# Kernel optimization log

Hardware: AMD Instinct MI355X
Metric: run time of the kernel (lower is better)

## Reference

```python
import jax, jax.numpy as jnp
import numpy as np

B, N, C, H = 8, 1024, 1024, 16


def setup_inputs() -> dict:
    key = jax.random.key(0)
    k1, k2, k3 = jax.random.split(key, 3)
    x = jax.random.normal(k1, (B, N, C), dtype=jnp.float32)
    # torch Linear weights stored pre-transposed as [in, out]
    w_qkv = jax.random.normal(k2, (C, 3 * C), dtype=jnp.float32) * (1.0 / np.sqrt(C))
    scale = jnp.ones((H, 1, 1), dtype=jnp.float32)
    w_out = jax.random.normal(k3, (C, C), dtype=jnp.float32) * (1.0 / np.sqrt(C))
    b_out = jnp.zeros((C,), dtype=jnp.float32)
    return {"x": x, "w_qkv": w_qkv, "scale": scale, "w_out": w_out, "b_out": b_out}


def _masked_softmax(dots, allow):
    # allow: [N, N] bool; True where attention is permitted (strictly lower triangle).
    neg = jnp.finfo(dots.dtype).min
    logits = jnp.where(allow, dots, neg)
    rowmax = jnp.max(logits, axis=-1, keepdims=True)
    unnorm = jnp.where(allow, jnp.exp(logits - rowmax), 0.0)
    denom = jnp.sum(unnorm, axis=-1, keepdims=True)
    # fully-masked rows (row 0) -> all-zero attention (flash-attn convention)
    return unnorm / jnp.where(denom == 0, 1.0, denom)


def reference(x, w_qkv, scale, w_out, b_out):
    b, n, c = x.shape
    h = scale.shape[0]
    d = c // h
    qkv = x @ w_qkv                                   # [B, N, 3C]
    q, k, v = jnp.split(qkv, 3, axis=-1)
    def heads(t):
        return t.reshape(b, n, h, d).transpose(0, 2, 1, 3)  # [B, H, N, D]
    q, k, v = heads(q), heads(k), heads(v)
    dots = jnp.einsum("bhnd,bhmd->bhnm", q, k) * scale     # per-head learnable scale
    # mask upper triangle AND the diagonal: allow only j < i
    allow = jnp.tril(jnp.ones((n, n), dtype=bool), k=-1)
    attn = _masked_softmax(dots, allow)
    out = jnp.einsum("bhnm,bhmd->bhnd", attn, v)           # [B, H, N, D]
    out = out.transpose(0, 2, 1, 3).reshape(b, n, c)
    return out @ w_out + b_out
```

## Files before the change

### kernel.cpp

```cpp
#include <hip/hip_runtime.h>

#define B_ 8
#define N_ 1024
#define C_ 1024
#define H_ 16
#define D_ 64

typedef __attribute__((ext_vector_type(8))) short short8v;
typedef __attribute__((ext_vector_type(4))) float f32x4;
typedef __attribute__((ext_vector_type(4))) unsigned short ushort4v;

__device__ __forceinline__ unsigned short f2bf_rne(float f) {
    unsigned int u = __float_as_uint(f);
    u += 0x7FFFu + ((u >> 16) & 1u);
    return (unsigned short)(u >> 16);
}
__device__ __forceinline__ float bf2f(unsigned short h) {
    return __uint_as_float(((unsigned int)h) << 16);
}

__global__ __launch_bounds__(256) void convert_transpose(
    const float* __restrict__ W, unsigned short* __restrict__ T_hi,
    unsigned short* __restrict__ T_lo, int K, int N)
{
    __shared__ float tile[32][33];
    const int nb = blockIdx.x * 32, kb = blockIdx.y * 32;
    const int t = threadIdx.x;
    {
        const int kr = t >> 3, nq = (t & 7) * 4;
        const float4 v = *(const float4*)&W[(size_t)(kb + kr) * N + nb + nq];
        tile[kr][nq + 0] = v.x; tile[kr][nq + 1] = v.y;
        tile[kr][nq + 2] = v.z; tile[kr][nq + 3] = v.w;
    }
    __syncthreads();
    {
        const int nr = t >> 3, kq = (t & 7) * 4;
        ushort4v hv, lv;
#pragma unroll
        for (int j = 0; j < 4; ++j) {
            const float f = tile[kq + j][nr];
            const unsigned short hu = f2bf_rne(f);
            hv[j] = hu;
            lv[j] = f2bf_rne(f - bf2f(hu));
        }
        const size_t o = (size_t)(nb + nr) * K + kb + kq;
        *(ushort4v*)&T_hi[o] = hv;
        *(ushort4v*)&T_lo[o] = lv;
    }
}

template<int A_F32>
__global__ __launch_bounds__(256, 2) void gemm_bf16x3(
    const void* __restrict__ Asrc, const unsigned short* __restrict__ Alo_src,
    const unsigned short* __restrict__ Bt_hi,
    const unsigned short* __restrict__ Bt_lo,
    const float* __restrict__ bias, float* __restrict__ Cmat,
    int M, int N, int K)
{
    __shared__ short As_hi[128 * 32], As_lo[128 * 32];
    __shared__ short Bs_hi[128 * 32], Bs_lo[128 * 32];

    const int tid = threadIdx.x;
    const int lane = tid & 63;
    const int wave = tid >> 6;
    const int wm = wave >> 1, wn = wave & 1;
    const int bm = blockIdx.y * 128, bn = blockIdx.x * 128;
    const int l15 = lane & 15, l4 = lane >> 4;

    f32x4 acc[4][4];
#pragma unroll
    for (int m = 0; m < 4; ++m)
#pragma unroll
        for (int n = 0; n < 4; ++n) acc[m][n] = (f32x4){0.f, 0.f, 0.f, 0.f};

    for (int k0 = 0; k0 < K; k0 += 32) {
        if (A_F32) {
            const float* A = (const float*)Asrc;
#pragma unroll
            for (int c = 0; c < 4; ++c) {
                const int u = tid + 256 * c;
                const int row = u >> 3, kc = u & 7;
                const float4 v = *(const float4*)&A[(size_t)(bm + row) * K + k0 + kc * 4];
                const float fv[4] = {v.x, v.y, v.z, v.w};
                ushort4v hv, lv;
#pragma unroll
                for (int j = 0; j < 4; ++j) {
                    const unsigned short hu = f2bf_rne(fv[j]);
                    hv[j] = hu;
                    lv[j] = f2bf_rne(fv[j] - bf2f(hu));
                }
                const int off = (row * 64 + kc * 8) ^ ((row & 7) << 4);
                *(ushort4v*)((char*)As_hi + off) = hv;
                *(ushort4v*)((char*)As_lo + off) = lv;
            }
        } else {
            const unsigned short* Ah = (const unsigned short*)Asrc;
#pragma unroll
            for (int c = 0; c < 2; ++c) {
                const int u = tid + 256 * c;
                const int row = u >> 2, kg = u & 3;
                const size_t gg = (size_t)(bm + row) * K + k0 + kg * 8;
                const int off = (row * 64 + kg * 16) ^ ((row & 7) << 4);
                *(short8v*)((char*)As_hi + off) = *(const short8v*)&Ah[gg];
                *(short8v*)((char*)As_lo + off) = *(const short8v*)&Alo_src[gg];
            }
        }
#pragma unroll
        for (int c = 0; c < 2; ++c) {
            const int u = tid + 256 * c;
            const int row = u >> 2, kg = u & 3;
            const size_t gg = (size_t)(bn + row) * K + k0 + kg * 8;
            const int off = (row * 64 + kg * 16) ^ ((row & 7) << 4);
            *(short8v*)((char*)Bs_hi + off) = *(const short8v*)&Bt_hi[gg];
            *(short8v*)((char*)Bs_lo + off) = *(const short8v*)&Bt_lo[gg];
        }
        __syncthreads();

        short8v ah[4], al[4], bh[4], bl[4];
#pragma unroll
        for (int m = 0; m < 4; ++m) {
            const int row = wm * 64 + m * 16 + l15;
            const int off = (row * 64 + l4 * 16) ^ ((row & 7) << 4);
            ah[m] = *(const short8v*)((char*)As_hi + off);
            al[m] = *(const short8v*)((char*)As_lo + off);
        }
#pragma unroll
        for (int n = 0; n < 4; ++n) {
            const int row = wn * 64 + n * 16 + l15;
            const int off = (row * 64 + l4 * 16) ^ ((row & 7) << 4);
            bh[n] = *(const short8v*)((char*)Bs_hi + off);
            bl[n] = *(const short8v*)((char*)Bs_lo + off);
        }

#pragma unroll
        for (int m = 0; m < 4; ++m)
#pragma unroll
            for (int n = 0; n < 4; ++n) {
                acc[m][n] = __builtin_amdgcn_mfma_f32_16x16x32_bf16(
                    ah[m], bh[n], acc[m][n], 0, 0, 0);
                acc[m][n] = __builtin_amdgcn_mfma_f32_16x16x32_bf16(
                    ah[m], bl[n], acc[m][n], 0, 0, 0);
                acc[m][n] = __builtin_amdgcn_mfma_f32_16x16x32_bf16(
                    al[m], bh[n], acc[m][n], 0, 0, 0);
            }
        __syncthreads();
    }

#pragma unroll
    for (int n = 0; n < 4; ++n) {
        const int col = bn + wn * 64 + n * 16 + l15;
        const float bv = bias ? bias[col] : 0.f;
#pragma unroll
        for (int m = 0; m < 4; ++m) {
            const int row0 = bm + wm * 64 + m * 16 + l4 * 4;
#pragma unroll
            for (int r = 0; r < 4; ++r)
                Cmat[(size_t)(row0 + r) * N + col] = acc[m][n][r] + bv;
        }
    }
}

__global__ __launch_bounds__(256, 2) void attn_mfma(
    const float* __restrict__ qkv, const float* __restrict__ scale,
    unsigned short* __restrict__ attn_hi, unsigned short* __restrict__ attn_lo)
{
    constexpr int C3 = 3 * C_;

    __shared__ short Kh[64 * 64];
    __shared__ short Kl[64 * 64];
    __shared__ short Vt[64 * 64];

    const int bid = blockIdx.x;
    const int rt  = 15 - (bid >> 7);
    const int hb  = bid & 127;
    const int h   = hb & 15;
    const int b   = hb >> 4;

    const int tid  = threadIdx.x;
    const int w    = tid >> 6;
    const int lane = tid & 63;
    const int l15  = lane & 15;
    const int g    = lane >> 4;

    const float sc = scale[h];

    short8v qh[2], ql[2];
    {
        const float* qrow =
            &qkv[((size_t)(b * N_ + rt * 64 + w * 16 + l15)) * C3 + h * D_];
#pragma unroll
        for (int t = 0; t < 2; ++t) {
            const float4 f0 = *(const float4*)&qrow[t * 32 + g * 8];
            const float4 f1 = *(const float4*)&qrow[t * 32 + g * 8 + 4];
            const float fv[8] = {f0.x, f0.y, f0.z, f0.w, f1.x, f1.y, f1.z, f1.w};
            union { short8v v; unsigned short u[8]; } H, L;
#pragma unroll
            for (int j = 0; j < 8; ++j) {
                const float f = fv[j] * sc;
                const unsigned short hu = f2bf_rne(f);
                H.u[j] = hu;
                L.u[j] = f2bf_rne(f - bf2f(hu));
            }
            qh[t] = H.v; ql[t] = L.v;
        }
    }

    f32x4 accO[4];
#pragma unroll
    for (int n = 0; n < 4; ++n) accO[n] = (f32x4){0.f, 0.f, 0.f, 0.f};
    float m_old = -1e30f, l_old = 0.f;

    for (int jt = 0; jt <= rt; ++jt) {
        __syncthreads();

#pragma unroll
        for (int it = 0; it < 4; ++it) {
            const int u2  = tid + 256 * it;
            const int row = u2 >> 4;
            const int dq  = (u2 & 15) * 4;
            const float* base =
                &qkv[((size_t)(b * N_ + jt * 64 + row)) * C3 + h * D_ + dq];
            const float4 kv = *(const float4*)(base + C_);
            const float kf[4] = {kv.x, kv.y, kv.z, kv.w};
            ushort4v kh4, kl4;
#pragma unroll
            for (int j = 0; j < 4; ++j) {
                const unsigned short hu = f2bf_rne(kf[j]);
                kh4[j] = hu;
                kl4[j] = f2bf_rne(kf[j] - bf2f(hu));
            }
            const int kbyte = (row * 128 + dq * 2) ^ ((row & 7) << 4);
            *(ushort4v*)((char*)Kh + kbyte) = kh4;
            *(ushort4v*)((char*)Kl + kbyte) = kl4;

            const float4 vv = *(const float4*)(base + 2 * C_);
            const float ov[4] = {vv.x, vv.y, vv.z, vv.w};
            float pvv[4];
#pragma unroll
            for (int j = 0; j < 4; ++j) pvv[j] = __shfl_xor(ov[j], 16, 64);
            const int row2 = row & ~1;
            const int odd  = row & 1;
#pragma unroll
            for (int s2 = 0; s2 < 2; ++s2) {
                const int i = odd * 2 + s2;
                const int d = dq + i;
                const float fe = odd ? pvv[i] : ov[i];
                const float fo = odd ? ov[i] : pvv[i];
                const unsigned int pack =
                    (unsigned int)f2bf_rne(fe) | ((unsigned int)f2bf_rne(fo) << 16);
                const int vbyte = (d * 128 + row2 * 2) ^ ((d & 7) << 4);
                *(unsigned int*)((char*)Vt + vbyte) = pack;
            }
        }
        __syncthreads();

        const int kbmax = (jt == rt) ? w : 3;
        f32x4 accS[4];
#pragma unroll
        for (int kb = 0; kb < 4; ++kb) accS[kb] = (f32x4){0.f, 0.f, 0.f, 0.f};
        for (int kb = 0; kb <= kbmax; ++kb) {
#pragma unroll
            for (int t = 0; t < 2; ++t) {
                const int kbyte =
                    ((16 * kb + l15) * 128 + t * 64 + g * 16) ^ ((l15 & 7) << 4);
                const short8v kh = *(const short8v*)((const char*)Kh + kbyte);
                const short8v kl = *(const short8v*)((const char*)Kl + kbyte);
                accS[kb] = __builtin_amdgcn_mfma_f32_16x16x32_bf16(
                    kh, qh[t], accS[kb], 0, 0, 0);
                accS[kb] = __builtin_amdgcn_mfma_f32_16x16x32_bf16(
                    kh, ql[t], accS[kb], 0, 0, 0);
                accS[kb] = __builtin_amdgcn_mfma_f32_16x16x32_bf16(
                    kl, qh[t], accS[kb], 0, 0, 0);
            }
        }

        float p[16];
        float tmax = -1e30f;
#pragma unroll
        for (int kb = 0; kb < 4; ++kb) {
#pragma unroll
            for (int r = 0; r < 4; ++r) {
                float s = accS[kb][r];
                bool allow = (kb <= kbmax);
                if (jt == rt && kb == w) allow = allow && ((4 * g + r) < l15);
                s = allow ? s : -1e30f;
                p[kb * 4 + r] = s;
                tmax = fmaxf(tmax, s);
            }
        }
        tmax = fmaxf(tmax, __shfl_xor(tmax, 16, 64));
        tmax = fmaxf(tmax, __shfl_xor(tmax, 32, 64));
        const float m_new = fmaxf(m_old, tmax);
        const float alpha = __expf(m_old - m_new);
        float lsum = 0.f;
#pragma unroll
        for (int i = 0; i < 16; ++i) {
            const float pe = (p[i] > -1e29f) ? __expf(p[i] - m_new) : 0.f;
            p[i] = pe;
            lsum += pe;
        }
        lsum += __shfl_xor(lsum, 16, 64);
        lsum += __shfl_xor(lsum, 32, 64);
        l_old = alpha * l_old + lsum;
        m_old = m_new;

        unsigned int pk[4][2];
#pragma unroll
        for (int kb = 0; kb < 4; ++kb) {
            pk[kb][0] = (unsigned int)f2bf_rne(p[kb * 4 + 0]) |
                        ((unsigned int)f2bf_rne(p[kb * 4 + 1]) << 16);
            pk[kb][1] = (unsigned int)f2bf_rne(p[kb * 4 + 2]) |
                        ((unsigned int)f2bf_rne(p[kb * 4 + 3]) << 16);
        }

        float ar[4];
#pragma unroll
        for (int r = 0; r < 4; ++r) ar[r] = __shfl(alpha, 4 * g + r, 64);
#pragma unroll
        for (int n = 0; n < 4; ++n)
#pragma unroll
            for (int r = 0; r < 4; ++r) accO[n][r] *= ar[r];

        const int s0 = l15 + 16 * ((2 * g) & 3);
        const int s1 = l15 + 16 * ((2 * g + 1) & 3);
        const bool lowg = (g < 2);
#pragma unroll
        for (int t = 0; t < 2; ++t) {
            const int a0 = __shfl((int)pk[2 * t][0], s0, 64);
            const int a1 = __shfl((int)pk[2 * t][1], s0, 64);
            const int b0 = __shfl((int)pk[2 * t + 1][0], s0, 64);
            const int b1 = __shfl((int)pk[2 * t + 1][1], s0, 64);
            const int c0 = __shfl((int)pk[2 * t][0], s1, 64);
            const int c1 = __shfl((int)pk[2 * t][1], s1, 64);
            const int d0 = __shfl((int)pk[2 * t + 1][0], s1, 64);
            const int d1 = __shfl((int)pk[2 * t + 1][1], s1, 64);
            union { short8v v; int u[4]; } A;
            A.u[0] = lowg ? a0 : b0;
            A.u[1] = lowg ? a1 : b1;
            A.u[2] = lowg ? c0 : d0;
            A.u[3] = lowg ? c1 : d1;
#pragma unroll
            for (int n = 0; n < 4; ++n) {
                const int vbyte =
                    ((16 * n + l15) * 128 + t * 64 + g * 16) ^ ((l15 & 7) << 4);
                const short8v vt = *(const short8v*)((const char*)Vt + vbyte);
                accO[n] = __builtin_amdgcn_mfma_f32_16x16x32_bf16(
                    A.v, vt, accO[n], 0, 0, 0);
            }
        }
    }

    float linv[4];
#pragma unroll
    for (int r = 0; r < 4; ++r) {
        const float lr = __shfl(l_old, 4 * g + r, 64);
        linv[r] = (lr > 0.f) ? 1.f / lr : 0.f;
    }
#pragma unroll
    for (int n = 0; n < 4; ++n) {
#pragma unroll
        for (int r = 0; r < 4; ++r) {
            const float f = accO[n][r] * linv[r];
            const unsigned short hu = f2bf_rne(f);
            const unsigned short lu = f2bf_rne(f - bf2f(hu));
            const size_t idx =
                ((size_t)(b * N_ + rt * 64 + w * 16 + 4 * g + r)) * C_ +
                h * 64 + 16 * n + l15;
            attn_hi[idx] = hu;
            attn_lo[idx] = lu;
        }
    }
}

extern "C" void kernel_launch(void* const* d_in, const int* in_sizes, int n_in,
                              void* d_out, int out_size, void* d_ws, size_t ws_size,
                              hipStream_t stream) {
    (void)in_sizes; (void)n_in; (void)out_size; (void)ws_size;
    const float* x      = (const float*)d_in[0];
    const float* w_qkv  = (const float*)d_in[1];
    const float* scale  = (const float*)d_in[2];
    const float* w_out  = (const float*)d_in[3];
    const float* b_out  = (const float*)d_in[4];
    float* out = (float*)d_out;

    char* ws = (char*)d_ws;
    float* qkv = (float*)ws;
    unsigned short* woutT_hi = (unsigned short*)ws;
    unsigned short* woutT_lo = (unsigned short*)(ws + ((size_t)2 << 20));
    unsigned short* wqkvT_hi = (unsigned short*)(ws + ((size_t)96 << 20));
    unsigned short* wqkvT_lo = (unsigned short*)(ws + ((size_t)102 << 20));
    unsigned short* attn_hi  = (unsigned short*)(ws + ((size_t)96 << 20));
    unsigned short* attn_lo  = (unsigned short*)(ws + ((size_t)112 << 20));

    const int M = B_ * N_;

    convert_transpose<<<dim3(3 * C_ / 32, C_ / 32), 256, 0, stream>>>(
        w_qkv, wqkvT_hi, wqkvT_lo, C_, 3 * C_);

    gemm_bf16x3<1><<<dim3(3 * C_ / 128, M / 128), 256, 0, stream>>>(
        x, nullptr, wqkvT_hi, wqkvT_lo, nullptr, qkv, M, 3 * C_, C_);

    attn_mfma<<<2048, 256, 0, stream>>>(qkv, scale, attn_hi, attn_lo);

    convert_transpose<<<dim3(C_ / 32, C_ / 32), 256, 0, stream>>>(
        w_out, woutT_hi, woutT_lo, C_, C_);

    gemm_bf16x3<0><<<dim3(C_ / 128, M / 128), 256, 0, stream>>>(
        attn_hi, attn_lo, woutT_hi, woutT_lo, b_out, out, M, C_, C_);
}
```

Measured before the change: 487.5 us.

## Pre-split activations to bf16 hi/lo and use direct global-to-LDS loads in GEMM

Adds a pass that splits x into bf16 hi/lo before the QKV GEMM, and makes the QKV GEMM write qkv directly as bf16 hi/lo pairs instead of fp32. The attention kernel then loads the pre-split Q/K/V without converting, reads only the hi part of V, and applies the per-head scale to the scores instead of to Q. Both GEMMs now stage tiles with global_load_lds 16-byte loads using an inverse-swizzle address map, skipping the register round trip. The cost is an extra split kernel and staging x_hi/x_lo in the output buffer. V losing its low part and the changed scale placement slightly alter precision.

```diff
diff --git a/kernel.cpp b/kernel.cpp
--- a/kernel.cpp
+++ b/kernel.cpp
@@ -17,6 +17,37 @@
 }
 __device__ __forceinline__ float bf2f(unsigned short h) {
     return __uint_as_float(((unsigned int)h) << 16);
+}
+
+__device__ __forceinline__ void gload16(const void* g, void* l) {
+    __builtin_amdgcn_global_load_lds(
+        (const __attribute__((address_space(1))) void*)g,
+        (__attribute__((address_space(3))) void*)l, 16, 0, 0);
+}
+
+__device__ __forceinline__ int inv_swz(int p) {
+    int l = p ^ ((p >> 2) & 0x40);
+    l ^= ((l >> 6) & 3) << 4;
+    return l;
+}
+
+__global__ __launch_bounds__(256) void split_f32(
+    const float* __restrict__ in, unsigned short* __restrict__ hi,
+    unsigned short* __restrict__ lo, int n4)
+{
+    for (int i = blockIdx.x * 256 + threadIdx.x; i < n4; i += gridDim.x * 256) {
+        const float4 v = *(const float4*)&in[(size_t)i * 4];
+        const float f[4] = {v.x, v.y, v.z, v.w};
+        ushort4v hv, lv;
+#pragma unroll
+        for (int j = 0; j < 4; ++j) {
+            const unsigned short hu = f2bf_rne(f[j]);
+            hv[j] = hu;
+            lv[j] = f2bf_rne(f[j] - bf2f(hu));
+        }
+        *(ushort4v*)&hi[(size_t)i * 4] = hv;
+        *(ushort4v*)&lo[(size_t)i * 4] = lv;
+    }
 }
 
 __global__ __launch_bounds__(256) void convert_transpose(
@@ -49,12 +80,12 @@
     }
 }
 
-template<int A_F32>
-__global__ __launch_bounds__(256, 2) void gemm_bf16x3(
-    const void* __restrict__ Asrc, const unsigned short* __restrict__ Alo_src,
-    const unsigned short* __restrict__ Bt_hi,
-    const unsigned short* __restrict__ Bt_lo,
-    const float* __restrict__ bias, float* __restrict__ Cmat,
+template<int OUT_SPLIT>
+__global__ __launch_bounds__(256, 2) void gemm_split(
+    const unsigned short* __restrict__ A_hi, const unsigned short* __restrict__ A_lo,
+    const unsigned short* __restrict__ Bt_hi, const unsigned short* __restrict__ Bt_lo,
+    const float* __restrict__ bias, float* __restrict__ Cf,
+    unsigned short* __restrict__ C_hi, unsigned short* __restrict__ C_lo,
     int M, int N, int K)
 {
     __shared__ short As_hi[128 * 32], As_lo[128 * 32];
@@ -62,11 +93,28 @@
 
     const int tid = threadIdx.x;
     const int lane = tid & 63;
-    const int wave = tid >> 6;
-    const int wm = wave >> 1, wn = wave & 1;
+    const int w = tid >> 6;
+    const int wm = w >> 1, wn = w & 1;
     const int bm = blockIdx.y * 128, bn = blockIdx.x * 128;
     const int l15 = lane & 15, l4 = lane >> 4;
 
+    const unsigned short *pAh[2], *pAl[2], *pBh[2], *pBl[2];
+    char *dAh[2], *dAl[2], *dBh[2], *dBl[2];
+#pragma unroll
+    for (int i = 0; i < 2; ++i) {
+        const int p = w * 2048 + i * 1024 + lane * 16;
+        const int l = inv_swz(p);
+        const int row = l >> 6, kg = (l >> 4) & 3;
+        pAh[i] = A_hi + (size_t)(bm + row) * K + kg * 8;
+        pAl[i] = A_lo + (size_t)(bm + row) * K + kg * 8;
+        pBh[i] = Bt_hi + (size_t)(bn + row) * K + kg * 8;
+        pBl[i] = Bt_lo + (size_t)(bn + row) * K + kg * 8;
+        dAh[i] = (char*)As_hi + w * 2048 + i * 1024;
+        dAl[i] = (char*)As_lo + w * 2048 + i * 1024;
+        dBh[i] = (char*)Bs_hi + w * 2048 + i * 1024;
+        dBl[i] = (char*)Bs_lo + w * 2048 + i * 1024;
+    }
+
     f32x4 acc[4][4];
 #pragma unroll
     for (int m = 0; m < 4; ++m)
@@ -74,45 +122,12 @@
         for (int n = 0; n < 4; ++n) acc[m][n] = (f32x4){0.f, 0.f, 0.f, 0.f};
 
     for (int k0 = 0; k0 < K; k0 += 32) {
-        if (A_F32) {
-            const float* A = (const float*)Asrc;
-#pragma unroll
-            for (int c = 0; c < 4; ++c) {
-                const int u = tid + 256 * c;
-                const int row = u >> 3, kc = u & 7;
-                const float4 v = *(const float4*)&A[(size_t)(bm + row) * K + k0 + kc * 4];
-                const float fv[4] = {v.x, v.y, v.z, v.w};
-                ushort4v hv, lv;
-#pragma unroll
-                for (int j = 0; j < 4; ++j) {
-                    const unsigned short hu = f2bf_rne(fv[j]);
-                    hv[j] = hu;
-                    lv[j] = f2bf_rne(fv[j] - bf2f(hu));
-                }
-                const int off = (row * 64 + kc * 8) ^ ((row & 7) << 4);
-                *(ushort4v*)((char*)As_hi + off) = hv;
-                *(ushort4v*)((char*)As_lo + off) = lv;
-            }
-        } else {
-            const unsigned short* Ah = (const unsigned short*)Asrc;
-#pragma unroll
-            for (int c = 0; c < 2; ++c) {
-                const int u = tid + 256 * c;
-                const int row = u >> 2, kg = u & 3;
-                const size_t gg = (size_t)(bm + row) * K + k0 + kg * 8;
-                const int off = (row * 64 + kg * 16) ^ ((row & 7) << 4);
-                *(short8v*)((char*)As_hi + off) = *(const short8v*)&Ah[gg];
-                *(short8v*)((char*)As_lo + off) = *(const short8v*)&Alo_src[gg];
-            }
-        }
-#pragma unroll
-        for (int c = 0; c < 2; ++c) {
-            const int u = tid + 256 * c;
-            const int row = u >> 2, kg = u & 3;
-            const size_t gg = (size_t)(bn + row) * K + k0 + kg * 8;
-            const int off = (row * 64 + kg * 16) ^ ((row & 7) << 4);
-            *(short8v*)((char*)Bs_hi + off) = *(const short8v*)&Bt_hi[gg];
-            *(short8v*)((char*)Bs_lo + off) = *(const short8v*)&Bt_lo[gg];
+#pragma unroll
+        for (int i = 0; i < 2; ++i) {
+            gload16(pAh[i] + k0, dAh[i]);
+            gload16(pAl[i] + k0, dAl[i]);
+            gload16(pBh[i] + k0, dBh[i]);
+            gload16(pBl[i] + k0, dBl[i]);
         }
         __syncthreads();
 
@@ -149,19 +164,30 @@
 #pragma unroll
     for (int n = 0; n < 4; ++n) {
         const int col = bn + wn * 64 + n * 16 + l15;
-        const float bv = bias ? bias[col] : 0.f;
+        const float bv = (!OUT_SPLIT && bias) ? bias[col] : 0.f;
 #pragma unroll
         for (int m = 0; m < 4; ++m) {
             const int row0 = bm + wm * 64 + m * 16 + l4 * 4;
 #pragma unroll
-            for (int r = 0; r < 4; ++r)
-                Cmat[(size_t)(row0 + r) * N + col] = acc[m][n][r] + bv;
+            for (int r = 0; r < 4; ++r) {
+                const size_t idx = (size_t)(row0 + r) * N + col;
+                if (OUT_SPLIT) {
+                    const float f = acc[m][n][r];
+                    const unsigned short hu = f2bf_rne(f);
+                    C_hi[idx] = hu;
+                    C_lo[idx] = f2bf_rne(f - bf2f(hu));
+                } else {
+                    Cf[idx] = acc[m][n][r] + bv;
+                }
+            }
         }
     }
 }
 
 __global__ __launch_bounds__(256, 2) void attn_mfma(
-    const float* __restrict__ qkv, const float* __restrict__ scale,
+    const unsigned short* __restrict__ qkv_hi,
+    const unsigned short* __restrict__ qkv_lo,
+    const float* __restrict__ scale,
     unsigned short* __restrict__ attn_hi, unsigned short* __restrict__ attn_lo)
 {
     constexpr int C3 = 3 * C_;
@@ -186,22 +212,12 @@
 
     short8v qh[2], ql[2];
     {
-        const float* qrow =
-            &qkv[((size_t)(b * N_ + rt * 64 + w * 16 + l15)) * C3 + h * D_];
+        const size_t qoff =
+            ((size_t)(b * N_ + rt * 64 + w * 16 + l15)) * C3 + h * D_;
 #pragma unroll
         for (int t = 0; t < 2; ++t) {
-            const float4 f0 = *(const float4*)&qrow[t * 32 + g * 8];
-            const float4 f1 = *(const float4*)&qrow[t * 32 + g * 8 + 4];
-            const float fv[8] = {f0.x, f0.y, f0.z, f0.w, f1.x, f1.y, f1.z, f1.w};
-            union { short8v v; unsigned short u[8]; } H, L;
-#pragma unroll
-            for (int j = 0; j < 8; ++j) {
-                const float f = fv[j] * sc;
-                const unsigned short hu = f2bf_rne(f);
-                H.u[j] = hu;
-                L.u[j] = f2bf_rne(f - bf2f(hu));
-            }
-            qh[t] = H.v; ql[t] = L.v;
+            qh[t] = *(const short8v*)&qkv_hi[qoff + t * 32 + g * 8];
+            ql[t] = *(const short8v*)&qkv_lo[qoff + t * 32 + g * 8];
         }
     }
 
@@ -214,40 +230,41 @@
         __syncthreads();
 
 #pragma unroll
-        for (int it = 0; it < 4; ++it) {
+        for (int it = 0; it < 2; ++it) {
             const int u2  = tid + 256 * it;
+            const int row = u2 >> 3;
+            const int dq8 = u2 & 7;
+            const size_t base =
+                ((size_t)(b * N_ + jt * 64 + row)) * C3 + C_ + h * D_ + dq8 * 8;
+            const int kbyte = (row * 128 + dq8 * 16) ^ ((row & 7) << 4);
+            *(short8v*)((char*)Kh + kbyte) = *(const short8v*)&qkv_hi[base];
+            *(short8v*)((char*)Kl + kbyte) = *(const short8v*)&qkv_lo[base];
+        }
+#pragma unroll
+        for (int vt = 0; vt < 4; ++vt) {
+            const int u2  = tid + 256 * vt;
             const int row = u2 >> 4;
             const int dq  = (u2 & 15) * 4;
-            const float* base =
-                &qkv[((size_t)(b * N_ + jt * 64 + row)) * C3 + h * D_ + dq];
-            const float4 kv = *(const float4*)(base + C_);
-            const float kf[4] = {kv.x, kv.y, kv.z, kv.w};
-            ushort4v kh4, kl4;
-#pragma unroll
-            for (int j = 0; j < 4; ++j) {
-                const unsigned short hu = f2bf_rne(kf[j]);
-                kh4[j] = hu;
-                kl4[j] = f2bf_rne(kf[j] - bf2f(hu));
-            }
-            const int kbyte = (row * 128 + dq * 2) ^ ((row & 7) << 4);
-            *(ushort4v*)((char*)Kh + kbyte) = kh4;
-            *(ushort4v*)((char*)Kl + kbyte) = kl4;
-
-            const float4 vv = *(const float4*)(base + 2 * C_);
-            const float ov[4] = {vv.x, vv.y, vv.z, vv.w};
-            float pvv[4];
-#pragma unroll
-            for (int j = 0; j < 4; ++j) pvv[j] = __shfl_xor(ov[j], 16, 64);
+            const size_t base =
+                ((size_t)(b * N_ + jt * 64 + row)) * C3 + 2 * C_ + h * D_ + dq;
+            const unsigned long long v8 = *(const unsigned long long*)&qkv_hi[base];
+            unsigned short ov[4];
+            ov[0] = (unsigned short)v8;
+            ov[1] = (unsigned short)(v8 >> 16);
+            ov[2] = (unsigned short)(v8 >> 32);
+            ov[3] = (unsigned short)(v8 >> 48);
+            int pv[4];
+#pragma unroll
+            for (int j = 0; j < 4; ++j) pv[j] = __shfl_xor((int)ov[j], 16, 64);
             const int row2 = row & ~1;
             const int odd  = row & 1;
 #pragma unroll
             for (int s2 = 0; s2 < 2; ++s2) {
                 const int i = odd * 2 + s2;
                 const int d = dq + i;
-                const float fe = odd ? pvv[i] : ov[i];
-                const float fo = odd ? ov[i] : pvv[i];
-                const unsigned int pack =
-                    (unsigned int)f2bf_rne(fe) | ((unsigned int)f2bf_rne(fo) << 16);
+                const unsigned int fe = odd ? (unsigned short)pv[i] : ov[i];
+                const unsigned int fo = odd ? ov[i] : (unsigned short)pv[i];
+                const unsigned int pack = fe | (fo << 16);
                 const int vbyte = (d * 128 + row2 * 2) ^ ((d & 7) << 4);
                 *(unsigned int*)((char*)Vt + vbyte) = pack;
             }
@@ -280,7 +297,7 @@
         for (int kb = 0; kb < 4; ++kb) {
 #pragma unroll
             for (int r = 0; r < 4; ++r) {
-                float s = accS[kb][r];
+                float s = accS[kb][r] * sc;
                 bool allow = (kb <= kbmax);
                 if (jt == rt && kb == w) allow = allow && ((4 * g + r) < l15);
                 s = allow ? s : -1e30f;
@@ -384,7 +401,10 @@
     float* out = (float*)d_out;
 
     char* ws = (char*)d_ws;
-    float* qkv = (float*)ws;
+    unsigned short* x_hi = (unsigned short*)d_out;
+    unsigned short* x_lo = x_hi + (size_t)B_ * N_ * C_;
+    unsigned short* qkv_hi = (unsigned short*)ws;
+    unsigned short* qkv_lo = (unsigned short*)(ws + ((size_t)48 << 20));
     unsigned short* woutT_hi = (unsigned short*)ws;
     unsigned short* woutT_lo = (unsigned short*)(ws + ((size_t)2 << 20));
     unsigned short* wqkvT_hi = (unsigned short*)(ws + ((size_t)96 << 20));
@@ -394,17 +414,21 @@
 
     const int M = B_ * N_;
 
+    split_f32<<<2048, 256, 0, stream>>>(x, x_hi, x_lo, M * C_ / 4);
+
     convert_transpose<<<dim3(3 * C_ / 32, C_ / 32), 256, 0, stream>>>(
         w_qkv, wqkvT_hi, wqkvT_lo, C_, 3 * C_);
 
-    gemm_bf16x3<1><<<dim3(3 * C_ / 128, M / 128), 256, 0, stream>>>(
-        x, nullptr, wqkvT_hi, wqkvT_lo, nullptr, qkv, M, 3 * C_, C_);
-
-    attn_mfma<<<2048, 256, 0, stream>>>(qkv, scale, attn_hi, attn_lo);
+    gemm_split<1><<<dim3(3 * C_ / 128, M / 128), 256, 0, stream>>>(
+        x_hi, x_lo, wqkvT_hi, wqkvT_lo, nullptr,
+        nullptr, qkv_hi, qkv_lo, M, 3 * C_, C_);
+
+    attn_mfma<<<2048, 256, 0, stream>>>(qkv_hi, qkv_lo, scale, attn_hi, attn_lo);
 
     convert_transpose<<<dim3(C_ / 32, C_ / 32), 256, 0, stream>>>(
         w_out, woutT_hi, woutT_lo, C_, C_);
 
-    gemm_bf16x3<0><<<dim3(C_ / 128, M / 128), 256, 0, stream>>>(
-        attn_hi, attn_lo, woutT_hi, woutT_lo, b_out, out, M, C_, C_);
-}
+    gemm_split<0><<<dim3(C_ / 128, M / 128), 256, 0, stream>>>(
+        attn_hi, attn_lo, woutT_hi, woutT_lo, b_out,
+        out, nullptr, nullptr, M, C_, C_);
+}
```

Result: faster. 413.1 us (-15.3%).
